# Optimization experiments

Hardware: AMD Instinct MI355X
Metric: run time of the kernel (lower is better)

## Reference

```python
import jax, jax.numpy as jnp
import numpy as np

NUM_LAYERS = 6
NUM_HEADS = 8
HIDDEN = 512
GRID_N = 32                      # num_nodes = GRID_N**2 + 1 (encoder pads a global node)
SEQ = GRID_N * GRID_N + 1        # 1025
FFN_HIDDEN = 32 * ((int(2 * HIDDEN / 3) + 31) // 32)  # 352, SwiGLU rounding
BATCH = 8
EPS = 1e-5


def build_grid_mask():
    """4-neighbor grid adjacency + self loops, padded with an all-connected first row/col."""
    n = GRID_N
    idx = np.arange(n * n).reshape(n, n)
    A = np.zeros((n * n, n * n), dtype=bool)
    # horizontal edges
    a, b = idx[:, :-1].ravel(), idx[:, 1:].ravel()
    A[a, b] = True; A[b, a] = True
    # vertical edges
    a, b = idx[:-1, :].ravel(), idx[1:, :].ravel()
    A[a, b] = True; A[b, a] = True
    np.fill_diagonal(A, True)
    M = np.ones((n * n + 1, n * n + 1), dtype=bool)
    M[1:, 1:] = A
    return jnp.asarray(M)


def setup_inputs() -> dict:
    key = jax.random.key(0)
    ks = jax.random.split(key, 9)
    std = 0.02
    D, F, L = HIDDEN, FFN_HIDDEN, NUM_LAYERS
    return {
        "x": jax.random.normal(ks[0], (BATCH, SEQ, D), dtype=jnp.float32),
        "mask": build_grid_mask(),                                  # [SEQ, SEQ] bool
        "wqkv": jax.random.normal(ks[1], (L, 3 * D, D), jnp.float32) * std,
        "wo":   jax.random.normal(ks[2], (L, D, D), jnp.float32) * std,
        "w1":   jax.random.normal(ks[3], (L, F, D), jnp.float32) * std,
        "w2":   jax.random.normal(ks[4], (L, D, F), jnp.float32) * std,
        "w3":   jax.random.normal(ks[5], (L, F, D), jnp.float32) * std,
        "attn_norm_w": jnp.ones((L, D), jnp.float32),
        "ffn_norm_w":  jnp.ones((L, D), jnp.float32),
    }


def rmsnorm(x, w):
    ms = jnp.mean(x * x, axis=-1, keepdims=True)
    return x * jax.lax.rsqrt(ms + EPS) * w


def reference(x, mask, wqkv, wo, w1, w2, w3, attn_norm_w, ffn_norm_w):
    B, S, D = x.shape
    H = NUM_HEADS
    hd = D // H
    scale = 1.0 / jnp.sqrt(jnp.asarray(hd, x.dtype))
    neg = jnp.asarray(-jnp.inf, x.dtype)
    for l in range(NUM_LAYERS):
        # --- attention ---
        h = rmsnorm(x, attn_norm_w[l])
        qkv = h @ wqkv[l].T                                   # [B,S,3D]
        q, k, v = jnp.split(qkv, 3, axis=-1)
        q = q.reshape(B, S, H, hd).transpose(0, 2, 1, 3)      # [B,H,S,hd]
        k = k.reshape(B, S, H, hd).transpose(0, 2, 1, 3)
        v = v.reshape(B, S, H, hd).transpose(0, 2, 1, 3)
        scores = jnp.einsum("bhqd,bhkd->bhqk", q, k) * scale  # [B,H,S,S]
        scores = jnp.where(mask, scores, neg)
        attn = jax.nn.softmax(scores, axis=-1)
        o = jnp.einsum("bhqk,bhkd->bhqd", attn, v)
        o = o.transpose(0, 2, 1, 3).reshape(B, S, D)
        x = x + o @ wo[l].T
        # --- SwiGLU FFN ---
        h = rmsnorm(x, ffn_norm_w[l])
        y = (jax.nn.silu(h @ w1[l].T) * (h @ w3[l].T)) @ w2[l].T
        x = x + y
    return x
```

## Files before the change

### kernel.cpp

```cpp
#include <hip/hip_runtime.h>

typedef unsigned short u16;
typedef short s8v __attribute__((ext_vector_type(8)));
typedef float f4v __attribute__((ext_vector_type(4)));

#define SEQ 1025
#define BATCH 8
#define MROWS (BATCH * SEQ)
#define D 512
#define TD 1536
#define F 352
#define F2I 768
#define FPAD 384
#define NLAYERS 6
#define QKVS ((size_t)BATCH * 8 * SEQ * 64)
#define EPS 132

__device__ __forceinline__ u16 f2b(float f) {
    unsigned u;
    __builtin_memcpy(&u, &f, 4);
    unsigned r = u + 0x7fffu + ((u >> 16) & 1u);
    return (u16)(r >> 16);
}
__device__ __forceinline__ float b2f(u16 h) {
    unsigned u = ((unsigned)h) << 16;
    float f;
    __builtin_memcpy(&f, &u, 4);
    return f;
}
__device__ __forceinline__ float rs_of(float ssq) {
    return rsqrtf(ssq * (1.0f / (float)D) + 1e-5f);
}

#define SEG0 (NLAYERS * TD * (D / 4))
#define SEG1 (SEG0 + NLAYERS * D * (D / 4))
#define SEG2 (SEG1 + NLAYERS * F2I * (D / 4))
#define SEG3 (SEG2 + NLAYERS * D * (FPAD / 4))
#define SEG4 (SEG3 + (12 * MROWS + 3) / 4)
__global__ __launch_bounds__(256) void convAll_k(const float* __restrict__ wqkv, const float* __restrict__ anw,
                                                 const float* __restrict__ wo,
                                                 const float* __restrict__ w1, const float* __restrict__ w3,
                                                 const float* __restrict__ fnw,
                                                 const float* __restrict__ w2,
                                                 u16* __restrict__ wqkvb, u16* __restrict__ wob,
                                                 u16* __restrict__ w13b, u16* __restrict__ w2b,
                                                 float* __restrict__ ssqz) {
    int i = blockIdx.x * 256 + threadIdx.x;
    if (i < SEG0) {
        int k4 = i & 127;
        int rem = i >> 7;
        int l = rem / TD;
        float4 v = ((const float4*)wqkv)[i];
        float4 w = ((const float4*)(anw + (size_t)l * D))[k4];
        ushort4 r;
        r.x = f2b(v.x * w.x); r.y = f2b(v.y * w.y); r.z = f2b(v.z * w.z); r.w = f2b(v.w * w.w);
        ((ushort4*)wqkvb)[i] = r;
    } else if (i < SEG1) {
        int j = i - SEG0;
        float4 v = ((const float4*)wo)[j];
        ushort4 r;
        r.x = f2b(v.x); r.y = f2b(v.y); r.z = f2b(v.z); r.w = f2b(v.w);
        ((ushort4*)wob)[j] = r;
    } else if (i < SEG2) {
        int j = i - SEG1;
        int k4 = j & 127;
        int rem = j >> 7;
        int n = rem % F2I, l = rem / F2I;
        int k32 = n >> 5, jj = n & 31;
        int f = k32 * 16 + (jj & 15);
        ushort4 r;
        if (f < F) {
            const float* src = (jj < 16) ? (w1 + ((size_t)(l * F + f) * D))
                                         : (w3 + ((size_t)(l * F + f) * D));
            float4 v = ((const float4*)src)[k4];
            float4 w = ((const float4*)(fnw + (size_t)l * D))[k4];
            r.x = f2b(v.x * w.x); r.y = f2b(v.y * w.y); r.z = f2b(v.z * w.z); r.w = f2b(v.w * w.w);
        } else {
            r.x = 0; r.y = 0; r.z = 0; r.w = 0;
        }
        ((ushort4*)w13b)[j] = r;
    } else if (i < SEG3) {
        int j = i - SEG2;
        int k4 = j % (FPAD / 4);
        int rem = j / (FPAD / 4);
        int n = rem % D, l = rem / D;
        ushort4 r;
        if (k4 < F / 4) {
            float4 v = ((const float4*)(w2 + (size_t)(l * D + n) * F))[k4];
            r.x = f2b(v.x); r.y = f2b(v.y); r.z = f2b(v.z); r.w = f2b(v.w);
        } else {
            r.x = 0; r.y = 0; r.z = 0; r.w = 0;
        }
        ((ushort4*)w2b)[j] = r;
    } else if (i < SEG4) {
        int j = i - SEG3;
        float4 z = {0.f, 0.f, 0.f, 0.f};
        if ((j + 1) * 4 <= 12 * MROWS) ((float4*)ssqz)[j] = z;
        else {
            for (int t = j * 4; t < 12 * MROWS; ++t) ssqz[t] = 0.f;
        }
    }
}

__global__ __launch_bounds__(128) void init_k(const float* __restrict__ xin, float* __restrict__ x,
                                              u16* __restrict__ xb, float* __restrict__ ssq0) {
    int row = blockIdx.x;
    int tid = threadIdx.x;
    float4 v = ((const float4*)(xin + (size_t)row * D))[tid];
    ((float4*)(x + (size_t)row * D))[tid] = v;
    ushort4 pk;
    pk.x = f2b(v.x); pk.y = f2b(v.y); pk.z = f2b(v.z); pk.w = f2b(v.w);
    ((ushort4*)(xb + (size_t)row * D))[tid] = pk;
    float ss = v.x * v.x + v.y * v.y + v.z * v.z + v.w * v.w;
    #pragma unroll
    for (int off = 32; off; off >>= 1) ss += __shfl_xor(ss, off);
    __shared__ float red[2];
    if ((tid & 63) == 0) red[tid >> 6] = ss;
    __syncthreads();
    if (tid == 0) ssq0[row] = red[0] + red[1];
}

#define STAGE_GEMM(bufofs, kk)                                                          \
    do {                                                                                \
        int k0_ = (kk);                                                                 \
        _Pragma("unroll")                                                               \
        for (int i_ = 0; i_ < 4; ++i_) {                                                \
            int chunk_ = i_ * 256 + tid;                                                \
            int row_ = chunk_ >> 3, kc_ = chunk_ & 7;                                   \
            int gr_ = tm + row_;                                                        \
            gr_ = gr_ < MROWS ? gr_ : MROWS - 1;                                        \
            const u16* srcA_ = A + (size_t)gr_ * K + k0_ + ((kc_ ^ (row_ & 7)) << 3);   \
            __builtin_amdgcn_global_load_lds(                                           \
                (const __attribute__((address_space(1))) void*)srcA_,                   \
                (__attribute__((address_space(3))) void*)(smem + (bufofs) + (size_t)chunk_ * 8), \
                16, 0, 0);                                                              \
            const u16* srcB_ = B + (size_t)(tn + row_) * K + k0_ + ((kc_ ^ (row_ & 7)) << 3); \
            __builtin_amdgcn_global_load_lds(                                           \
                (const __attribute__((address_space(1))) void*)srcB_,                   \
                (__attribute__((address_space(3))) void*)(smem + 16384 + (bufofs) + (size_t)chunk_ * 8), \
                16, 0, 0);                                                              \
        }                                                                               \
    } while (0)

template <int MODE, int K, int LDC, int NX, int NWG>
__global__ __launch_bounds__(256) void gemm_bt_k(const u16* __restrict__ A, const u16* __restrict__ B,
                                                 void* __restrict__ C, const float* __restrict__ ssqIn,
                                                 float* __restrict__ ssqOut, u16* __restrict__ xb) {
    __shared__ u16 smem[34048];
    const int tid = threadIdx.x;
    const int lane = tid & 63;
    const int wave = tid >> 6;
    int hw = blockIdx.x;
    constexpr int q8 = NWG >> 3, r8 = NWG & 7;
    int xcd = hw & 7, pos = hw >> 3;
    int work = (xcd < r8 ? xcd * (q8 + 1) : r8 * (q8 + 1) + (xcd - r8) * q8) + pos;
    int ty = work / NX, tx = work - ty * NX;
    const int tm = ty * 128;
    const int tn = tx * 128;
    const int wm = (wave >> 1) * 64;
    const int wn = (wave & 1) * 64;
    f4v acc[4][4] = {};

    constexpr int nk = K >> 6;
    STAGE_GEMM(0, 0);
    __syncthreads();
    #pragma unroll
    for (int k = 0; k < nk; ++k) {
        int cur = (k & 1) * 8192;
        if (k + 1 < nk) STAGE_GEMM(cur ^ 8192, (k + 1) << 6);
        const u16* sa_ = smem + cur;
        const u16* sb_ = smem + 16384 + cur;
        #pragma unroll
        for (int ks = 0; ks < 2; ++ks) {
            int kc = ks * 4 + (lane >> 4);
            s8v af[4], bfr[4];
            #pragma unroll
            for (int mi = 0; mi < 4; ++mi) {
                int row = wm + mi * 16 + (lane & 15);
                af[mi] = *(const s8v*)(sa_ + row * 64 + ((kc ^ (row & 7)) << 3));
            }
            #pragma unroll
            for (int ni = 0; ni < 4; ++ni) {
                int row = wn + ni * 16 + (lane & 15);
                bfr[ni] = *(const s8v*)(sb_ + row * 64 + ((kc ^ (row & 7)) << 3));
            }
            #pragma unroll
            for (int mi = 0; mi < 4; ++mi)
                #pragma unroll
                for (int ni = 0; ni < 4; ++ni)
                    acc[mi][ni] = __builtin_amdgcn_mfma_f32_16x16x32_bf16(af[mi], bfr[ni], acc[mi][ni], 0, 0, 0);
        }
        __syncthreads();
    }

    float* ldsf = (float*)smem;
    #pragma unroll
    for (int mi = 0; mi < 4; ++mi)
        #pragma unroll
        for (int ni = 0; ni < 4; ++ni)
            #pragma unroll
            for (int rr = 0; rr < 4; ++rr) {
                int r = wm + mi * 16 + ((lane >> 4) << 2) + rr;
                int c = wn + ni * 16 + (lane & 15);
                ldsf[r * EPS + c] = acc[mi][ni][rr];
            }
    __syncthreads();

    const int jj = tid & 7;
    #pragma unroll
    for (int pass = 0; pass < 4; ++pass) {
        int r = pass * 32 + (tid >> 3);
        int row = tm + r;
        if (row >= MROWS) continue;
        if (MODE == 1) {
            float sumsq = 0.f;
            #pragma unroll
            for (int i = 0; i < 4; ++i) {
                float4 v = *(float4*)&ldsf[r * EPS + i * 32 + jj * 4];
                int col = tn + i * 32 + jj * 4;
                float* p = (float*)C + (size_t)row * LDC + col;
                float4 o = *(float4*)p;
                o.x += v.x; o.y += v.y; o.z += v.z; o.w += v.w;
                *(float4*)p = o;
                ushort4 s;
                s.x = f2b(o.x); s.y = f2b(o.y); s.z = f2b(o.z); s.w = f2b(o.w);
                *(ushort4*)(xb + (size_t)row * D + col) = s;
                sumsq += o.x * o.x + o.y * o.y + o.z * o.z + o.w * o.w;
            }
            sumsq += __shfl_xor(sumsq, 1);
            sumsq += __shfl_xor(sumsq, 2);
            sumsq += __shfl_xor(sumsq, 4);
            if (jj == 0) atomicAdd(ssqOut + row, sumsq);
        } else if (MODE == 2) {
            float s_ = rs_of(ssqIn[row]);
            int b = row / SEQ, q = row - b * SEQ;
            #pragma unroll
            for (int i = 0; i < 4; ++i) {
                int col = tn + i * 32 + jj * 4;
                int part = col >> 9, h = (col >> 6) & 7, d = col & 63;
                float4 v = *(float4*)&ldsf[r * EPS + i * 32 + jj * 4];
                ushort4 s;
                s.x = f2b(v.x * s_); s.y = f2b(v.y * s_); s.z = f2b(v.z * s_); s.w = f2b(v.w * s_);
                *(ushort4*)((u16*)C + (size_t)part * QKVS + (((size_t)(b * 8 + h)) * SEQ + q) * 64 + d) = s;
            }
        } else {
            float s_ = rs_of(ssqIn[row]);
            #pragma unroll
            for (int i = 0; i < 4; ++i) {
                float a0 = ldsf[r * EPS + i * 32 + jj * 2] * s_;
                float a1 = ldsf[r * EPS + i * 32 + jj * 2 + 1] * s_;
                float b0 = ldsf[r * EPS + i * 32 + 16 + jj * 2] * s_;
                float b1 = ldsf[r * EPS + i * 32 + 16 + jj * 2 + 1] * s_;
                float g0 = a0 / (1.f + __expf(-a0)) * b0;
                float g1 = a1 / (1.f + __expf(-a1)) * b1;
                int f = (tn >> 1) + i * 16 + jj * 2;
                unsigned pk = (unsigned)f2b(g0) | ((unsigned)f2b(g1) << 16);
                *(unsigned*)((u16*)C + (size_t)row * FPAD + f) = pk;
            }
        }
    }
}

__global__ __launch_bounds__(256) void attn_k(const u16* __restrict__ qt, const u16* __restrict__ kt,
                                              const u16* __restrict__ vt, u16* __restrict__ o) {
    const int tid = threadIdx.x;
    if (blockIdx.x >= 64) {
        int sid = blockIdx.x - 64;
        int qtile = sid & 7, bh = sid >> 3;
        int h = bh & 7, b = bh >> 3;
        const size_t slab = (size_t)bh * SEQ * 64;
        const int ql = tid >> 1, half = tid & 1;
        const int q = 1 + qtile * 128 + ql;
        const int q1 = q - 1, r = q1 >> 5, c = q1 & 31;

        const u16* qp = qt + slab + (size_t)q * 64 + half * 32;
        float qf[32];
        #pragma unroll
        for (int cc = 0; cc < 4; ++cc) {
            s8v qv = *(const s8v*)(qp + cc * 8);
            #pragma unroll
            for (int i = 0; i < 8; ++i) qf[cc * 8 + i] = b2f((u16)qv[i]);
        }
        int key[6]; bool valid[6];
        key[0] = 0;      valid[0] = true;
        key[1] = q;      valid[1] = true;
        key[2] = q - 1;  valid[2] = (c > 0);
        key[3] = q + 1;  valid[3] = (c < 31);
        key[4] = q - 32; valid[4] = (r > 0);
        key[5] = q + 32; valid[5] = (r < 31);

        float sc[6];
        #pragma unroll
        for (int j = 0; j < 6; ++j) {
            int kk = valid[j] ? key[j] : 0;
            const u16* kp = kt + slab + (size_t)kk * 64 + half * 32;
            float d = 0.f;
            #pragma unroll
            for (int cc = 0; cc < 4; ++cc) {
                s8v kv = *(const s8v*)(kp + cc * 8);
                #pragma unroll
                for (int i = 0; i < 8; ++i) d += qf[cc * 8 + i] * b2f((u16)kv[i]);
            }
            d += __shfl_xor(d, 1);
            sc[j] = valid[j] ? d * 0.125f : -1e30f;
        }
        float m = sc[0];
        #pragma unroll
        for (int j = 1; j < 6; ++j) m = fmaxf(m, sc[j]);
        float w[6], l = 0.f;
        #pragma unroll
        for (int j = 0; j < 6; ++j) { w[j] = __expf(sc[j] - m); l += w[j]; }
        float inv = 1.f / l;

        float acc[32];
        #pragma unroll
        for (int i = 0; i < 32; ++i) acc[i] = 0.f;
        #pragma unroll
        for (int j = 0; j < 6; ++j) {
            int kk = valid[j] ? key[j] : 0;
            const u16* vp = vt + slab + (size_t)kk * 64 + half * 32;
            #pragma unroll
            for (int cc = 0; cc < 4; ++cc) {
                s8v vv = *(const s8v*)(vp + cc * 8);
                #pragma unroll
                for (int i = 0; i < 8; ++i) acc[cc * 8 + i] += w[j] * b2f((u16)vv[i]);
            }
        }
        u16* orow = o + ((size_t)b * SEQ + q) * D + h * 64 + half * 32;
        #pragma unroll
        for (int cc = 0; cc < 4; ++cc) {
            uint4 pk;
            pk.x = (unsigned)f2b(acc[cc * 8 + 0] * inv) | ((unsigned)f2b(acc[cc * 8 + 1] * inv) << 16);
            pk.y = (unsigned)f2b(acc[cc * 8 + 2] * inv) | ((unsigned)f2b(acc[cc * 8 + 3] * inv) << 16);
            pk.z = (unsigned)f2b(acc[cc * 8 + 4] * inv) | ((unsigned)f2b(acc[cc * 8 + 5] * inv) << 16);
            pk.w = (unsigned)f2b(acc[cc * 8 + 6] * inv) | ((unsigned)f2b(acc[cc * 8 + 7] * inv) << 16);
            *(uint4*)(orow + cc * 8) = pk;
        }
    } else {
        __shared__ float sp[SEQ + 15];
        __shared__ float red[8];
        __shared__ float sacc[4][64];
        int bh = blockIdx.x;
        int h = bh & 7, b = bh >> 3;
        const size_t slab = (size_t)bh * SEQ * 64;
        const int lane = tid & 63, wv = tid >> 6;

        float qf[64];
        #pragma unroll
        for (int cc = 0; cc < 8; ++cc) {
            s8v qv = *(const s8v*)(qt + slab + cc * 8);
            #pragma unroll
            for (int i = 0; i < 8; ++i) qf[cc * 8 + i] = b2f((u16)qv[i]);
        }
        for (int j0 = tid; j0 < SEQ; j0 += 256) {
            const u16* kp = kt + slab + (size_t)j0 * 64;
            float p0 = 0.f, p1 = 0.f, p2 = 0.f, p3 = 0.f;
            #pragma unroll
            for (int cc = 0; cc < 8; ++cc) {
                s8v kv = *(const s8v*)(kp + cc * 8);
                p0 += qf[cc * 8 + 0] * b2f((u16)kv[0]) + qf[cc * 8 + 4] * b2f((u16)kv[4]);
                p1 += qf[cc * 8 + 1] * b2f((u16)kv[1]) + qf[cc * 8 + 5] * b2f((u16)kv[5]);
                p2 += qf[cc * 8 + 2] * b2f((u16)kv[2]) + qf[cc * 8 + 6] * b2f((u16)kv[6]);
                p3 += qf[cc * 8 + 3] * b2f((u16)kv[3]) + qf[cc * 8 + 7] * b2f((u16)kv[7]);
            }
            sp[j0] = ((p0 + p1) + (p2 + p3)) * 0.125f;
        }
        __syncthreads();
        float m = -1e30f;
        for (int j = tid; j < SEQ; j += 256) m = fmaxf(m, sp[j]);
        #pragma unroll
        for (int off = 32; off; off >>= 1) m = fmaxf(m, __shfl_xor(m, off));
        if (lane == 0) red[wv] = m;
        __syncthreads();
        m = fmaxf(fmaxf(red[0], red[1]), fmaxf(red[2], red[3]));
        float lsum = 0.f;
        for (int j = tid; j < SEQ; j += 256) { float e = __expf(sp[j] - m); sp[j] = e; lsum += e; }
        #pragma unroll
        for (int off = 32; off; off >>= 1) lsum += __shfl_xor(lsum, off);
        if (lane == 0) red[4 + wv] = lsum;
        __syncthreads();
        float L = (red[4] + red[5]) + (red[6] + red[7]);
        const int quarter = lane & 3, stripe = lane >> 2;
        float acc[16];
        #pragma unroll
        for (int i = 0; i < 16; ++i) acc[i] = 0.f;
        const int jbase = wv * 256;
        const int njj = (wv == 3) ? 17 : 16;
        for (int jj2 = 0; jj2 < njj; ++jj2) {
            int j = jbase + jj2 * 16 + stripe;
            float wj = (j < SEQ) ? sp[j] : 0.f;
            int je = j < 1024 ? j : 1024;
            const u16* vp = vt + slab + (size_t)je * 64 + quarter * 16;
            s8v v0 = *(const s8v*)(vp);
            s8v v1 = *(const s8v*)(vp + 8);
            #pragma unroll
            for (int i = 0; i < 8; ++i) {
                acc[i]     += wj * b2f((u16)v0[i]);
                acc[8 + i] += wj * b2f((u16)v1[i]);
            }
        }
        #pragma unroll
        for (int off = 4; off <= 32; off <<= 1) {
            #pragma unroll
            for (int i = 0; i < 16; ++i) acc[i] += __shfl_xor(acc[i], off);
        }
        if (lane < 4) {
            #pragma unroll
            for (int i = 0; i < 16; ++i) sacc[wv][lane * 16 + i] = acc[i];
        }
        __syncthreads();
        if (tid < 64) {
            float A = (sacc[0][tid] + sacc[1][tid]) + (sacc[2][tid] + sacc[3][tid]);
            o[((size_t)b * SEQ) * D + h * 64 + tid] = f2b(A / L);
        }
    }
}

extern "C" void kernel_launch(void* const* d_in, const int* in_sizes, int n_in,
                              void* d_out, int out_size, void* d_ws, size_t ws_size,
                              hipStream_t stream) {
    const int M = MROWS;
    const float* x_in = (const float*)d_in[0];
    const float* wqkv = (const float*)d_in[2];
    const float* wo   = (const float*)d_in[3];
    const float* w1   = (const float*)d_in[4];
    const float* w2   = (const float*)d_in[5];
    const float* w3   = (const float*)d_in[6];
    const float* anw  = (const float*)d_in[7];
    const float* fnw  = (const float*)d_in[8];
    float* x = (float*)d_out;

    char* ws = (char*)d_ws;
    auto alloc = [&](size_t n) { char* p = ws; ws += (n + 255) & ~(size_t)255; return p; };
    u16* qkvt  = (u16*)alloc(3 * QKVS * 2);
    u16* xb    = (u16*)alloc((size_t)M * D * 2);
    u16* ob    = (u16*)alloc((size_t)M * D * 2);
    float* ssqs = (float*)alloc((size_t)13 * M * 4);
    u16* wqkvb = (u16*)alloc((size_t)NLAYERS * TD * D * 2);
    u16* wob   = (u16*)alloc((size_t)NLAYERS * D * D * 2);
    u16* w13b  = (u16*)alloc((size_t)NLAYERS * F2I * D * 2);
    u16* w2b   = (u16*)alloc((size_t)NLAYERS * D * FPAD * 2);
    u16* gp = qkvt;

    convAll_k<<<(SEG4 + 255) / 256, 256, 0, stream>>>(wqkv, anw, wo, w1, w3, fnw, w2,
                                                      wqkvb, wob, w13b, w2b, ssqs + M);
    init_k<<<M, 128, 0, stream>>>(x_in, x, xb, ssqs);

    constexpr int mt = (MROWS + 127) / 128;
    constexpr int gQKV = mt * (TD / 128);
    constexpr int gD   = mt * (D / 128);
    constexpr int gF   = mt * (F2I / 128);
    for (int l = 0; l < NLAYERS; ++l) {
        float* ssqPrev = ssqs + (size_t)(2 * l) * M;
        float* ssqA    = ssqs + (size_t)(2 * l + 1) * M;
        float* ssqB    = ssqs + (size_t)(2 * l + 2) * M;
        gemm_bt_k<2, 512, TD, TD / 128, gQKV><<<gQKV, 256, 0, stream>>>(
            xb, wqkvb + (size_t)l * TD * D, qkvt, ssqPrev, nullptr, nullptr);
        attn_k<<<64 + 512, 256, 0, stream>>>(qkvt, qkvt + QKVS, qkvt + 2 * QKVS, ob);
        gemm_bt_k<1, 512, D, D / 128, gD><<<gD, 256, 0, stream>>>(
            ob, wob + (size_t)l * D * D, x, nullptr, ssqA, xb);
        gemm_bt_k<3, 512, FPAD, F2I / 128, gF><<<gF, 256, 0, stream>>>(
            xb, w13b + (size_t)l * F2I * D, gp, ssqA, nullptr, nullptr);
        gemm_bt_k<1, 384, D, D / 128, gD><<<gD, 256, 0, stream>>>(
            gp, w2b + (size_t)l * D * FPAD, x, nullptr, ssqB, xb);
    }
}
```

Baseline: 510.2 us.

## Use 128x64 tiles for residual GEMMs and fold init into conversion kernel

Adds a dedicated GEMM kernel with 128x64 output tiles for the two D=512-wide residual projections (attention output and FFN down). This doubles the workgroup count so more of the GPU's compute units stay busy on these small-N GEMMs. The init kernel is merged into the weight-conversion kernel to save one launch. The trade-off is that each A tile is now loaded twice as often, and per-wave MFMA work is smaller relative to the LDS traffic.

```diff
diff --git a/kernel.cpp b/kernel.cpp
--- a/kernel.cpp
+++ b/kernel.cpp
@@ -15,6 +15,7 @@
 #define NLAYERS 6
 #define QKVS ((size_t)BATCH * 8 * SEQ * 64)
 #define EPS 132
+#define EPS64 68
 
 __device__ __forceinline__ u16 f2b(float f) {
     unsigned u;
@@ -36,7 +37,8 @@
 #define SEG1 (SEG0 + NLAYERS * D * (D / 4))
 #define SEG2 (SEG1 + NLAYERS * F2I * (D / 4))
 #define SEG3 (SEG2 + NLAYERS * D * (FPAD / 4))
-#define SEG4 (SEG3 + (12 * MROWS + 3) / 4)
+#define SEG4P (SEG3 + ((12 * MROWS / 4 + 255) & ~255))
+#define SEG5 (SEG4P + MROWS * 128)
 __global__ __launch_bounds__(256) void convAll_k(const float* __restrict__ wqkv, const float* __restrict__ anw,
                                                  const float* __restrict__ wo,
                                                  const float* __restrict__ w1, const float* __restrict__ w3,
@@ -44,7 +46,9 @@
                                                  const float* __restrict__ w2,
                                                  u16* __restrict__ wqkvb, u16* __restrict__ wob,
                                                  u16* __restrict__ w13b, u16* __restrict__ w2b,
-                                                 float* __restrict__ ssqz) {
+                                                 float* __restrict__ ssqz,
+                                                 const float* __restrict__ xin, float* __restrict__ x,
+                                                 u16* __restrict__ xb, float* __restrict__ ssq0) {
     int i = blockIdx.x * 256 + threadIdx.x;
     if (i < SEG0) {
         int k4 = i & 127;
@@ -92,32 +96,30 @@
             r.x = 0; r.y = 0; r.z = 0; r.w = 0;
         }
         ((ushort4*)w2b)[j] = r;
-    } else if (i < SEG4) {
+    } else if (i < SEG4P) {
         int j = i - SEG3;
-        float4 z = {0.f, 0.f, 0.f, 0.f};
-        if ((j + 1) * 4 <= 12 * MROWS) ((float4*)ssqz)[j] = z;
-        else {
-            for (int t = j * 4; t < 12 * MROWS; ++t) ssqz[t] = 0.f;
-        }
-    }
-}
-
-__global__ __launch_bounds__(128) void init_k(const float* __restrict__ xin, float* __restrict__ x,
-                                              u16* __restrict__ xb, float* __restrict__ ssq0) {
-    int row = blockIdx.x;
-    int tid = threadIdx.x;
-    float4 v = ((const float4*)(xin + (size_t)row * D))[tid];
-    ((float4*)(x + (size_t)row * D))[tid] = v;
-    ushort4 pk;
-    pk.x = f2b(v.x); pk.y = f2b(v.y); pk.z = f2b(v.z); pk.w = f2b(v.w);
-    ((ushort4*)(xb + (size_t)row * D))[tid] = pk;
-    float ss = v.x * v.x + v.y * v.y + v.z * v.z + v.w * v.w;
-    #pragma unroll
-    for (int off = 32; off; off >>= 1) ss += __shfl_xor(ss, off);
-    __shared__ float red[2];
-    if ((tid & 63) == 0) red[tid >> 6] = ss;
-    __syncthreads();
-    if (tid == 0) ssq0[row] = red[0] + red[1];
+        if (j < 12 * MROWS / 4) {
+            float4 z = {0.f, 0.f, 0.f, 0.f};
+            ((float4*)ssqz)[j] = z;
+        }
+    } else if (i < SEG5) {
+        int j = i - SEG4P;
+        int row = j >> 7, t = j & 127;
+        int tid = threadIdx.x;
+        float4 v = ((const float4*)(xin + (size_t)row * D))[t];
+        ((float4*)(x + (size_t)row * D))[t] = v;
+        ushort4 pk;
+        pk.x = f2b(v.x); pk.y = f2b(v.y); pk.z = f2b(v.z); pk.w = f2b(v.w);
+        ((ushort4*)(xb + (size_t)row * D))[t] = pk;
+        float ss = v.x * v.x + v.y * v.y + v.z * v.z + v.w * v.w;
+        #pragma unroll
+        for (int off = 32; off; off >>= 1) ss += __shfl_xor(ss, off);
+        __shared__ float red[4];
+        if ((tid & 63) == 0) red[tid >> 6] = ss;
+        __syncthreads();
+        if (tid == 0) ssq0[row] = red[0] + red[1];
+        if (tid == 128) ssq0[row] = red[2] + red[3];
+    }
 }
 
 #define STAGE_GEMM(bufofs, kk)                                                          \
@@ -212,26 +214,7 @@
         int r = pass * 32 + (tid >> 3);
         int row = tm + r;
         if (row >= MROWS) continue;
-        if (MODE == 1) {
-            float sumsq = 0.f;
-            #pragma unroll
-            for (int i = 0; i < 4; ++i) {
-                float4 v = *(float4*)&ldsf[r * EPS + i * 32 + jj * 4];
-                int col = tn + i * 32 + jj * 4;
-                float* p = (float*)C + (size_t)row * LDC + col;
-                float4 o = *(float4*)p;
-                o.x += v.x; o.y += v.y; o.z += v.z; o.w += v.w;
-                *(float4*)p = o;
-                ushort4 s;
-                s.x = f2b(o.x); s.y = f2b(o.y); s.z = f2b(o.z); s.w = f2b(o.w);
-                *(ushort4*)(xb + (size_t)row * D + col) = s;
-                sumsq += o.x * o.x + o.y * o.y + o.z * o.z + o.w * o.w;
-            }
-            sumsq += __shfl_xor(sumsq, 1);
-            sumsq += __shfl_xor(sumsq, 2);
-            sumsq += __shfl_xor(sumsq, 4);
-            if (jj == 0) atomicAdd(ssqOut + row, sumsq);
-        } else if (MODE == 2) {
+        if (MODE == 2) {
             float s_ = rs_of(ssqIn[row]);
             int b = row / SEQ, q = row - b * SEQ;
             #pragma unroll
@@ -258,6 +241,125 @@
                 *(unsigned*)((u16*)C + (size_t)row * FPAD + f) = pk;
             }
         }
+    }
+}
+
+template <int K, int NWG>
+__global__ __launch_bounds__(256) void gemm_bt64_k(const u16* __restrict__ A, const u16* __restrict__ B,
+                                                   float* __restrict__ C,
+                                                   float* __restrict__ ssqOut, u16* __restrict__ xb) {
+    __shared__ u16 smem[24576];
+    const int tid = threadIdx.x;
+    const int lane = tid & 63;
+    const int wave = tid >> 6;
+    int hw = blockIdx.x;
+    constexpr int q8 = NWG >> 3, r8 = NWG & 7;
+    int xcd = hw & 7, pos = hw >> 3;
+    int work = (xcd < r8 ? xcd * (q8 + 1) : r8 * (q8 + 1) + (xcd - r8) * q8) + pos;
+    int ty = work >> 3, tx = work & 7;
+    const int tm = ty * 128;
+    const int tn = tx * 64;
+    const int wm = (wave >> 1) * 64;
+    const int wn = (wave & 1) * 32;
+    f4v acc[4][2] = {};
+
+    constexpr int nk = K >> 6;
+#define STAGE64(cur_, kk)                                                               \
+    do {                                                                                \
+        int k0_ = (kk);                                                                 \
+        _Pragma("unroll")                                                               \
+        for (int i_ = 0; i_ < 4; ++i_) {                                                \
+            int chunk_ = i_ * 256 + tid;                                                \
+            int row_ = chunk_ >> 3, kc_ = chunk_ & 7;                                   \
+            int gr_ = tm + row_;                                                        \
+            gr_ = gr_ < MROWS ? gr_ : MROWS - 1;                                        \
+            const u16* srcA_ = A + (size_t)gr_ * K + k0_ + ((kc_ ^ (row_ & 7)) << 3);   \
+            __builtin_amdgcn_global_load_lds(                                           \
+                (const __attribute__((address_space(1))) void*)srcA_,                   \
+                (__attribute__((address_space(3))) void*)(smem + (cur_) * 8192 + (size_t)chunk_ * 8), \
+                16, 0, 0);                                                              \
+        }                                                                               \
+        _Pragma("unroll")                                                               \
+        for (int i_ = 0; i_ < 2; ++i_) {                                                \
+            int chunk_ = i_ * 256 + tid;                                                \
+            int row_ = chunk_ >> 3, kc_ = chunk_ & 7;                                   \
+            const u16* srcB_ = B + (size_t)(tn + row_) * K + k0_ + ((kc_ ^ (row_ & 7)) << 3); \
+            __builtin_amdgcn_global_load_lds(                                           \
+                (const __attribute__((address_space(1))) void*)srcB_,                   \
+                (__attribute__((address_space(3))) void*)(smem + 16384 + (cur_) * 4096 + (size_t)chunk_ * 8), \
+                16, 0, 0);                                                              \
+        }                                                                               \
+    } while (0)
+
+    STAGE64(0, 0);
+    __syncthreads();
+    #pragma unroll
+    for (int k = 0; k < nk; ++k) {
+        int cur = k & 1;
+        if (k + 1 < nk) STAGE64(cur ^ 1, (k + 1) << 6);
+        const u16* sa_ = smem + cur * 8192;
+        const u16* sb_ = smem + 16384 + cur * 4096;
+        #pragma unroll
+        for (int ks = 0; ks < 2; ++ks) {
+            int kc = ks * 4 + (lane >> 4);
+            s8v af[4], bfr[2];
+            #pragma unroll
+            for (int mi = 0; mi < 4; ++mi) {
+                int row = wm + mi * 16 + (lane & 15);
+                af[mi] = *(const s8v*)(sa_ + row * 64 + ((kc ^ (row & 7)) << 3));
+            }
+            #pragma unroll
+            for (int ni = 0; ni < 2; ++ni) {
+                int row = wn + ni * 16 + (lane & 15);
+                bfr[ni] = *(const s8v*)(sb_ + row * 64 + ((kc ^ (row & 7)) << 3));
+            }
+            #pragma unroll
+            for (int mi = 0; mi < 4; ++mi)
+                #pragma unroll
+                for (int ni = 0; ni < 2; ++ni)
+                    acc[mi][ni] = __builtin_amdgcn_mfma_f32_16x16x32_bf16(af[mi], bfr[ni], acc[mi][ni], 0, 0, 0);
+        }
+        __syncthreads();
+    }
+#undef STAGE64
+
+    float* ldsf = (float*)smem;
+    #pragma unroll
+    for (int mi = 0; mi < 4; ++mi)
+        #pragma unroll
+        for (int ni = 0; ni < 2; ++ni)
+            #pragma unroll
+            for (int rr = 0; rr < 4; ++rr) {
+                int r = wm + mi * 16 + ((lane >> 4) << 2) + rr;
+                int c = wn + ni * 16 + (lane & 15);
+                ldsf[r * EPS64 + c] = acc[mi][ni][rr];
+            }
+    __syncthreads();
+
+    const int jj = tid & 7;
+    #pragma unroll
+    for (int pass = 0; pass < 4; ++pass) {
+        int r = pass * 32 + (tid >> 3);
+        int row = tm + r;
+        if (row >= MROWS) continue;
+        float sumsq = 0.f;
+        #pragma unroll
+        for (int i = 0; i < 2; ++i) {
+            float4 v = *(float4*)&ldsf[r * EPS64 + i * 32 + jj * 4];
+            int col = tn + i * 32 + jj * 4;
+            float* p = C + (size_t)row * D + col;
+            float4 o = *(float4*)p;
+            o.x += v.x; o.y += v.y; o.z += v.z; o.w += v.w;
+            *(float4*)p = o;
+            ushort4 s;
+            s.x = f2b(o.x); s.y = f2b(o.y); s.z = f2b(o.z); s.w = f2b(o.w);
+            *(ushort4*)(xb + (size_t)row * D + col) = s;
+            sumsq += o.x * o.x + o.y * o.y + o.z * o.z + o.w * o.w;
+        }
+        sumsq += __shfl_xor(sumsq, 1);
+        sumsq += __shfl_xor(sumsq, 2);
+        sumsq += __shfl_xor(sumsq, 4);
+        if (jj == 0) atomicAdd(ssqOut + row, sumsq);
     }
 }
 
@@ -442,13 +544,13 @@
     u16* w2b   = (u16*)alloc((size_t)NLAYERS * D * FPAD * 2);
     u16* gp = qkvt;
 
-    convAll_k<<<(SEG4 + 255) / 256, 256, 0, stream>>>(wqkv, anw, wo, w1, w3, fnw, w2,
-                                                      wqkvb, wob, w13b, w2b, ssqs + M);
-    init_k<<<M, 128, 0, stream>>>(x_in, x, xb, ssqs);
+    convAll_k<<<(SEG5 + 255) / 256, 256, 0, stream>>>(wqkv, anw, wo, w1, w3, fnw, w2,
+                                                      wqkvb, wob, w13b, w2b, ssqs + M,
+                                                      x_in, x, xb, ssqs);
 
     constexpr int mt = (MROWS + 127) / 128;
     constexpr int gQKV = mt * (TD / 128);
-    constexpr int gD   = mt * (D / 128);
+    constexpr int gD64 = mt * (D / 64);
     constexpr int gF   = mt * (F2I / 128);
     for (int l = 0; l < NLAYERS; ++l) {
         float* ssqPrev = ssqs + (size_t)(2 * l) * M;
@@ -457,11 +559,11 @@
         gemm_bt_k<2, 512, TD, TD / 128, gQKV><<<gQKV, 256, 0, stream>>>(
             xb, wqkvb + (size_t)l * TD * D, qkvt, ssqPrev, nullptr, nullptr);
         attn_k<<<64 + 512, 256, 0, stream>>>(qkvt, qkvt + QKVS, qkvt + 2 * QKVS, ob);
-        gemm_bt_k<1, 512, D, D / 128, gD><<<gD, 256, 0, stream>>>(
-            ob, wob + (size_t)l * D * D, x, nullptr, ssqA, xb);
+        gemm_bt64_k<512, gD64><<<gD64, 256, 0, stream>>>(
+            ob, wob + (size_t)l * D * D, x, ssqA, xb);
         gemm_bt_k<3, 512, FPAD, F2I / 128, gF><<<gF, 256, 0, stream>>>(
             xb, w13b + (size_t)l * F2I * D, gp, ssqA, nullptr, nullptr);
-        gemm_bt_k<1, 384, D, D / 128, gD><<<gD, 256, 0, stream>>>(
-            gp, w2b + (size_t)l * D * FPAD, x, nullptr, ssqB, xb);
-    }
-}
+        gemm_bt64_k<384, gD64><<<gD64, 256, 0, stream>>>(
+            gp, w2b + (size_t)l * D * FPAD, x, ssqB, xb);
+    }
+}
```

Measured after the change: 495.9 us. 1.03x faster.
